# Kernel optimization log

Measured on AMD Instinct MI355X. Metric: run time of the kernel, lower is better.

## Reference

```python
import jax, jax.numpy as jnp
import numpy as np

LN_EPS = 1e-5


def _layernorm_hd(x, gamma, beta):
    # normalize jointly over the last two dims (H, D), matching nn.LayerNorm((H, D))
    m = jnp.mean(x, axis=(-2, -1), keepdims=True)
    v = jnp.var(x, axis=(-2, -1), keepdims=True)
    return (x - m) * jax.lax.rsqrt(v + LN_EPS) * gamma + beta


def setup_inputs() -> dict:
    B, S, H, D = 4, 4096, 8, 64
    key = jax.random.key(0)
    k1, k2, k3 = jax.random.split(key, 3)
    heads_input = jax.random.normal(k1, (B, S, H, D), dtype=jnp.float32)
    W_hid = jax.random.normal(k2, (2 * D, 3 * D), dtype=jnp.float32) * (1.0 / np.sqrt(2 * D))
    b_hid = jnp.zeros((3 * D,), dtype=jnp.float32)
    W_og = jax.random.normal(k3, (2 * D, D), dtype=jnp.float32) * (1.0 / np.sqrt(2 * D))
    b_og = jnp.zeros((D,), dtype=jnp.float32)
    ln_gamma = jnp.ones((H, D), dtype=jnp.float32)
    ln_beta = jnp.zeros((H, D), dtype=jnp.float32)
    init_cx = jnp.zeros((H, D), dtype=jnp.float32)
    return {"heads_input": heads_input, "W_hid": W_hid, "b_hid": b_hid,
            "W_og": W_og, "b_og": b_og, "ln_gamma": ln_gamma,
            "ln_beta": ln_beta, "init_cx": init_cx}


def reference(heads_input, W_hid, b_hid, W_og, b_og, ln_gamma, ln_beta, init_cx):
    B, S, H, D = heads_input.shape
    # RS1cumsumFunc: exclusive (right-shifted) cumsum along seq of detached input
    x_det = jax.lax.stop_gradient(heads_input)
    cs = jnp.cumsum(x_det, axis=1)
    csum_raw = jnp.concatenate([jnp.zeros_like(cs[:, :1]), cs[:, :-1]], axis=1)
    csum = _layernorm_hd(csum_raw, ln_gamma, ln_beta)

    # trans_hid on concat(heads_input, csum): [B,S,H,2D] -> [B,S,H,3D]
    hid_in = jnp.concatenate([heads_input, csum], axis=-1)
    h3 = jnp.einsum('bshd,de->bshe', hid_in, W_hid) + b_hid
    igate, fgate, hidden = jnp.split(h3, 3, axis=-1)
    fg = jax.nn.sigmoid(fgate)
    igh = jax.nn.sigmoid(igate) * jax.nn.relu(hidden)

    # LGateFunc: cell_t = fg_t * cell_{t-1} + igh_t, cell_{-1} = init_cx
    def combine(c1, c2):
        a1, b1 = c1
        a2, b2 = c2
        return a1 * a2, b1 * a2 + b2

    a, b = jax.lax.associative_scan(combine, (fg, igh), axis=1)
    cell = a * init_cx + b  # init_cx [H,D] broadcasts over [B,S,H,D]

    og_in = jnp.concatenate([heads_input, cell], axis=-1)
    og = jax.nn.sigmoid(jnp.einsum('bshd,de->bshe', og_in, W_og) + b_og)
    return og * cell
```

## Files before the change

### kernel.cpp

```cpp
#include <hip/hip_runtime.h>
#include <math.h>

#define S_   4096
#define H_   8
#define D_   64
#define HD_  512
#define NCH  256
#define LCH  16
#define RC   128

typedef __bf16 bf16x8 __attribute__((ext_vector_type(8)));
typedef float  f32x4  __attribute__((ext_vector_type(4)));

__device__ __forceinline__ float sigm(float v) { return 1.f / (1.f + __expf(-v)); }

__global__ __launch_bounds__(256) void k_wt(const float* __restrict__ Wh,
                                            const float* __restrict__ Wo,
                                            __bf16* __restrict__ Wth,
                                            __bf16* __restrict__ Wto) {
  int idx = blockIdx.x * 256 + threadIdx.x;
  if (idx < 24576) {
    int k = idx / 192, n = idx % 192;
    Wth[n * 128 + k] = (__bf16)Wh[idx];
  } else {
    int j = idx - 24576;
    int k = j >> 6, n = j & 63;
    Wto[n * 128 + k] = (__bf16)Wo[j];
  }
}

__global__ __launch_bounds__(512) void k_chunk_sums(const float* __restrict__ x,
                                                    float* __restrict__ sums) {
  const int b = blockIdx.x >> 8, c = blockIdx.x & 255;
  const int t = threadIdx.x;
  const float* p = x + ((size_t)b * S_ + c * LCH) * HD_ + t;
  float acc = 0.f;
  #pragma unroll
  for (int i = 0; i < LCH; ++i) acc += p[(size_t)i * HD_];
  sums[((size_t)b * NCH + c) * HD_ + t] = acc;
}

__global__ __launch_bounds__(512) void k_scan_offsets(float* __restrict__ sums) {
  const int b = blockIdx.x, t = threadIdx.x;
  float run = 0.f;
  for (int c = 0; c < NCH; ++c) {
    size_t idx = ((size_t)b * NCH + c) * HD_ + t;
    float v = sums[idx];
    sums[idx] = run;
    run += v;
  }
}

__global__ __launch_bounds__(512) void k_ln(const float* __restrict__ x,
                                            const float* __restrict__ offs,
                                            const float* __restrict__ gamma,
                                            const float* __restrict__ beta,
                                            __bf16* __restrict__ Abf) {
  __shared__ float2 red[2][8];
  const int b = blockIdx.x >> 8, c = blockIdx.x & 255;
  const int t = threadIdx.x;
  float run = offs[((size_t)b * NCH + c) * HD_ + t];
  const float g = gamma[t], be = beta[t];
  const size_t xbase = ((size_t)b * S_ + c * LCH) * HD_ + t;
  const int h = t >> 6, d = t & 63;
  float xv = x[xbase];
  for (int i = 0; i < LCH; ++i) {
    float xn = (i < LCH - 1) ? x[xbase + (size_t)(i + 1) * HD_] : 0.f;
    float v = run, v2 = run * run;
    #pragma unroll
    for (int o = 32; o; o >>= 1) { v += __shfl_xor(v, o); v2 += __shfl_xor(v2, o); }
    if ((t & 63) == 0) red[i & 1][t >> 6] = make_float2(v, v2);
    __syncthreads();
    float s1 = 0.f, s2 = 0.f;
    #pragma unroll
    for (int w = 0; w < 8; ++w) { s1 += red[i & 1][w].x; s2 += red[i & 1][w].y; }
    float m = s1 * (1.f / HD_);
    float var = fmaf(-m, m, s2 * (1.f / HD_));
    float inv = rsqrtf(var + 1e-5f);
    size_t r = ((size_t)b * S_ + c * LCH + i) * H_ + h;
    Abf[r * 128 + 64 + d] = (__bf16)((run - m) * inv * g + be);
    Abf[r * 128 + d] = (__bf16)xv;
    run += xv;
    xv = xn;
  }
}

__global__ __launch_bounds__(256) void k_gates(const __bf16* __restrict__ Abf,
                                               const __bf16* __restrict__ Wt,
                                               const float* __restrict__ bh,
                                               float* __restrict__ fg,
                                               float* __restrict__ igh,
                                               float* __restrict__ cA,
                                               float* __restrict__ cB) {
  __shared__ float fgl[RC * 68];
  __shared__ float ighl[RC * 68];
  const int t = threadIdx.x;
  const int wave = t >> 6, lane = t & 63;
  const int quad = lane >> 4, l16 = lane & 15;
  const int r0 = blockIdx.x * RC;

  f32x4 acc[2][12];
  #pragma unroll
  for (int i = 0; i < 2; ++i)
    #pragma unroll
    for (int j = 0; j < 12; ++j) acc[i][j] = (f32x4){0.f, 0.f, 0.f, 0.f};

  #pragma unroll
  for (int ks = 0; ks < 4; ++ks) {
    bf16x8 bfrag[12];
    #pragma unroll
    for (int nt = 0; nt < 12; ++nt)
      bfrag[nt] = *(const bf16x8*)(Wt + (nt * 16 + l16) * 128 + ks * 32 + quad * 8);
    #pragma unroll
    for (int mi = 0; mi < 2; ++mi) {
      int mt = wave * 2 + mi;
      bf16x8 afrag = *(const bf16x8*)(Abf + (size_t)(r0 + mt * 16 + l16) * 128 + ks * 32 + quad * 8);
      #pragma unroll
      for (int nt = 0; nt < 12; ++nt)
        acc[mi][nt] = __builtin_amdgcn_mfma_f32_16x16x32_bf16(afrag, bfrag[nt], acc[mi][nt], 0, 0, 0);
    }
  }

  #pragma unroll
  for (int mi = 0; mi < 2; ++mi) {
    int mt = wave * 2 + mi;
    #pragma unroll
    for (int nt = 0; nt < 4; ++nt) {
      int d = nt * 16 + l16;
      float bi = bh[d], bf = bh[64 + d], bhv = bh[128 + d];
      #pragma unroll
      for (int r = 0; r < 4; ++r) {
        int row = mt * 16 + quad * 4 + r;
        float ip = acc[mi][nt][r] + bi;
        float fp = acc[mi][nt + 4][r] + bf;
        float hp = acc[mi][nt + 8][r] + bhv;
        fgl[row * 68 + d] = sigm(fp);
        ighl[row * 68 + d] = sigm(ip) * fmaxf(hp, 0.f);
      }
    }
  }
  __syncthreads();

  #pragma unroll
  for (int rep = 0; rep < 8; ++rep) {
    int idx = rep * 256 + t;
    int row = idx >> 4, c4 = idx & 15;
    float4 vf = *(const float4*)&fgl[row * 68 + c4 * 4];
    float4 vg = *(const float4*)&ighl[row * 68 + c4 * 4];
    ((float4*)fg)[(size_t)(r0 + row) * 16 + c4] = vf;
    ((float4*)igh)[(size_t)(r0 + row) * 16 + c4] = vg;
  }

  #pragma unroll
  for (int p = 0; p < 2; ++p) {
    int hd = p * 256 + t;
    int h = hd >> 6, d = hd & 63;
    float a = 1.f, bb = 0.f;
    #pragma unroll
    for (int s = 0; s < LCH; ++s) {
      float f = fgl[(s * 8 + h) * 68 + d];
      float g = ighl[(s * 8 + h) * 68 + d];
      a *= f;
      bb = fmaf(bb, f, g);
    }
    cA[(size_t)blockIdx.x * 512 + hd] = a;
    cB[(size_t)blockIdx.x * 512 + hd] = bb;
  }
}

__global__ __launch_bounds__(512) void k_cell_scan(float* __restrict__ cA,
                                                   const float* __restrict__ cB,
                                                   const float* __restrict__ initcx) {
  const int b = blockIdx.x, t = threadIdx.x;
  float run = initcx[t];
  for (int c = 0; c < NCH; ++c) {
    size_t idx = ((size_t)b * NCH + c) * HD_ + t;
    float a = cA[idx], bb = cB[idx];
    cA[idx] = run;
    run = fmaf(a, run, bb);
  }
}

__global__ __launch_bounds__(256) void k_og(const __bf16* __restrict__ Abf,
                                            const float* __restrict__ fg,
                                            const float* __restrict__ igh,
                                            const float* __restrict__ cin,
                                            const __bf16* __restrict__ Wt,
                                            const float* __restrict__ bo,
                                            float* __restrict__ out) {
  __shared__ float cl[RC * 68];
  const int t = threadIdx.x;
  const int wave = t >> 6, lane = t & 63;
  const int quad = lane >> 4, l16 = lane & 15;
  const int r0 = blockIdx.x * RC;

  #pragma unroll
  for (int p = 0; p < 2; ++p) {
    int hd = p * 256 + t;
    int h = hd >> 6, d = hd & 63;
    float run = cin[(size_t)blockIdx.x * 512 + hd];
    #pragma unroll
    for (int s = 0; s < LCH; ++s) {
      size_t row = (size_t)r0 + s * 8 + h;
      run = fmaf(fg[row * 64 + d], run, igh[row * 64 + d]);
      cl[(s * 8 + h) * 68 + d] = run;
    }
  }
  __syncthreads();

  f32x4 acc[2][4];
  #pragma unroll
  for (int i = 0; i < 2; ++i)
    #pragma unroll
    for (int j = 0; j < 4; ++j) acc[i][j] = (f32x4){0.f, 0.f, 0.f, 0.f};

  #pragma unroll
  for (int ks = 0; ks < 4; ++ks) {
    bf16x8 bfrag[4];
    #pragma unroll
    for (int nt = 0; nt < 4; ++nt)
      bfrag[nt] = *(const bf16x8*)(Wt + (nt * 16 + l16) * 128 + ks * 32 + quad * 8);
    #pragma unroll
    for (int mi = 0; mi < 2; ++mi) {
      int mt = wave * 2 + mi;
      bf16x8 afrag;
      if (ks < 2) {
        afrag = *(const bf16x8*)(Abf + (size_t)(r0 + mt * 16 + l16) * 128 + ks * 32 + quad * 8);
      } else {
        int rowl = mt * 16 + l16;
        const float* src = &cl[rowl * 68 + (ks - 2) * 32 + quad * 8];
        #pragma unroll
        for (int j = 0; j < 8; ++j) afrag[j] = (__bf16)src[j];
      }
      #pragma unroll
      for (int nt = 0; nt < 4; ++nt)
        acc[mi][nt] = __builtin_amdgcn_mfma_f32_16x16x32_bf16(afrag, bfrag[nt], acc[mi][nt], 0, 0, 0);
    }
  }

  #pragma unroll
  for (int mi = 0; mi < 2; ++mi) {
    int mt = wave * 2 + mi;
    #pragma unroll
    for (int nt = 0; nt < 4; ++nt) {
      int d = nt * 16 + l16;
      float bv = bo[d];
      #pragma unroll
      for (int r = 0; r < 4; ++r) {
        int rowl = mt * 16 + quad * 4 + r;
        float og = sigm(acc[mi][nt][r] + bv);
        out[(size_t)(r0 + rowl) * 64 + d] = og * cl[rowl * 68 + d];
      }
    }
  }
}

extern "C" void kernel_launch(void* const* d_in, const int* in_sizes, int n_in,
                              void* d_out, int out_size, void* d_ws, size_t ws_size,
                              hipStream_t stream) {
  const float* x      = (const float*)d_in[0];
  const float* W_hid  = (const float*)d_in[1];
  const float* b_hid  = (const float*)d_in[2];
  const float* W_og   = (const float*)d_in[3];
  const float* b_og   = (const float*)d_in[4];
  const float* gamma  = (const float*)d_in[5];
  const float* beta   = (const float*)d_in[6];
  const float* initcx = (const float*)d_in[7];
  float* out = (float*)d_out;
  float* ws  = (float*)d_ws;

  float*  buf0 = ws;
  float*  buf1 = ws + 524288;
  __bf16* Abf  = (__bf16*)(ws + 1048576);
  float*  fgv  = ws + 1048576 + 8388608;
  float*  ighv = fgv + 8388608;
  __bf16* Wth  = (__bf16*)(ighv + 8388608);
  __bf16* Wto  = Wth + 24576;

  k_wt         <<<128,  256, 0, stream>>>(W_hid, W_og, Wth, Wto);
  k_chunk_sums <<<1024, 512, 0, stream>>>(x, buf0);
  k_scan_offsets<<<4,   512, 0, stream>>>(buf0);
  k_ln         <<<1024, 512, 0, stream>>>(x, buf0, gamma, beta, Abf);
  k_gates      <<<1024, 256, 0, stream>>>(Abf, Wth, b_hid, fgv, ighv, buf0, buf1);
  k_cell_scan  <<<4,    512, 0, stream>>>(buf0, buf1, initcx);
  k_og         <<<1024, 256, 0, stream>>>(Abf, fgv, ighv, buf0, Wto, b_og, out);
}
```

Measured before the change: 219.0 us.

## Recompute gates in output kernel instead of storing fg/igh to global memory

```diff
diff --git a/kernel.cpp b/kernel.cpp
--- a/kernel.cpp
+++ b/kernel.cpp
@@ -29,43 +29,49 @@
   }
 }
 
-__global__ __launch_bounds__(512) void k_chunk_sums(const float* __restrict__ x,
-                                                    float* __restrict__ sums) {
-  const int b = blockIdx.x >> 8, c = blockIdx.x & 255;
+__global__ __launch_bounds__(512) void k_pre(const float* __restrict__ x,
+                                             float* __restrict__ sums,
+                                             __bf16* __restrict__ Abf) {
   const int t = threadIdx.x;
-  const float* p = x + ((size_t)b * S_ + c * LCH) * HD_ + t;
+  const int h = t >> 6, d = t & 63;
+  const size_t r0 = (size_t)blockIdx.x * RC;
+  const float* p = x + r0 * 64 + t;
   float acc = 0.f;
   #pragma unroll
-  for (int i = 0; i < LCH; ++i) acc += p[(size_t)i * HD_];
-  sums[((size_t)b * NCH + c) * HD_ + t] = acc;
-}
-
-__global__ __launch_bounds__(512) void k_scan_offsets(float* __restrict__ sums) {
+  for (int i = 0; i < LCH; ++i) {
+    float v = p[(size_t)i * HD_];
+    acc += v;
+    Abf[(r0 + (size_t)i * H_ + h) * 128 + d] = (__bf16)v;
+  }
+  sums[(size_t)blockIdx.x * HD_ + t] = acc;
+}
+
+__global__ __launch_bounds__(512) void k_scan_offsets(const float* __restrict__ sums,
+                                                      float* __restrict__ offs) {
   const int b = blockIdx.x, t = threadIdx.x;
   float run = 0.f;
+  #pragma unroll 16
   for (int c = 0; c < NCH; ++c) {
     size_t idx = ((size_t)b * NCH + c) * HD_ + t;
     float v = sums[idx];
-    sums[idx] = run;
+    offs[idx] = run;
     run += v;
   }
 }
 
-__global__ __launch_bounds__(512) void k_ln(const float* __restrict__ x,
-                                            const float* __restrict__ offs,
+__global__ __launch_bounds__(512) void k_ln(const float* __restrict__ offs,
                                             const float* __restrict__ gamma,
                                             const float* __restrict__ beta,
                                             __bf16* __restrict__ Abf) {
   __shared__ float2 red[2][8];
-  const int b = blockIdx.x >> 8, c = blockIdx.x & 255;
   const int t = threadIdx.x;
-  float run = offs[((size_t)b * NCH + c) * HD_ + t];
+  const int h = t >> 6, d = t & 63;
+  const size_t r0 = (size_t)blockIdx.x * RC;
+  float run = offs[(size_t)blockIdx.x * HD_ + t];
   const float g = gamma[t], be = beta[t];
-  const size_t xbase = ((size_t)b * S_ + c * LCH) * HD_ + t;
-  const int h = t >> 6, d = t & 63;
-  float xv = x[xbase];
   for (int i = 0; i < LCH; ++i) {
-    float xn = (i < LCH - 1) ? x[xbase + (size_t)(i + 1) * HD_] : 0.f;
+    size_t row = r0 + (size_t)i * H_ + h;
+    float xv = (float)Abf[row * 128 + d];
     float v = run, v2 = run * run;
     #pragma unroll
     for (int o = 32; o; o >>= 1) { v += __shfl_xor(v, o); v2 += __shfl_xor(v2, o); }
@@ -77,27 +83,20 @@
     float m = s1 * (1.f / HD_);
     float var = fmaf(-m, m, s2 * (1.f / HD_));
     float inv = rsqrtf(var + 1e-5f);
-    size_t r = ((size_t)b * S_ + c * LCH + i) * H_ + h;
-    Abf[r * 128 + 64 + d] = (__bf16)((run - m) * inv * g + be);
-    Abf[r * 128 + d] = (__bf16)xv;
+    Abf[row * 128 + 64 + d] = (__bf16)((run - m) * inv * g + be);
     run += xv;
-    xv = xn;
   }
 }
 
 __global__ __launch_bounds__(256) void k_gates(const __bf16* __restrict__ Abf,
                                                const __bf16* __restrict__ Wt,
                                                const float* __restrict__ bh,
-                                               float* __restrict__ fg,
-                                               float* __restrict__ igh,
                                                float* __restrict__ cA,
                                                float* __restrict__ cB) {
-  __shared__ float fgl[RC * 68];
-  __shared__ float ighl[RC * 68];
   const int t = threadIdx.x;
   const int wave = t >> 6, lane = t & 63;
   const int quad = lane >> 4, l16 = lane & 15;
-  const int r0 = blockIdx.x * RC;
+  const size_t r0 = (size_t)blockIdx.x * RC;
 
   f32x4 acc[2][12];
   #pragma unroll
@@ -113,8 +112,8 @@
       bfrag[nt] = *(const bf16x8*)(Wt + (nt * 16 + l16) * 128 + ks * 32 + quad * 8);
     #pragma unroll
     for (int mi = 0; mi < 2; ++mi) {
-      int mt = wave * 2 + mi;
-      bf16x8 afrag = *(const bf16x8*)(Abf + (size_t)(r0 + mt * 16 + l16) * 128 + ks * 32 + quad * 8);
+      int h = wave * 2 + mi;
+      bf16x8 afrag = *(const bf16x8*)(Abf + (r0 + l16 * H_ + h) * 128 + ks * 32 + quad * 8);
       #pragma unroll
       for (int nt = 0; nt < 12; ++nt)
         acc[mi][nt] = __builtin_amdgcn_mfma_f32_16x16x32_bf16(afrag, bfrag[nt], acc[mi][nt], 0, 0, 0);
@@ -123,133 +122,159 @@
 
   #pragma unroll
   for (int mi = 0; mi < 2; ++mi) {
-    int mt = wave * 2 + mi;
+    int h = wave * 2 + mi;
     #pragma unroll
     for (int nt = 0; nt < 4; ++nt) {
       int d = nt * 16 + l16;
       float bi = bh[d], bf = bh[64 + d], bhv = bh[128 + d];
+      float A = 1.f, Bv = 0.f;
       #pragma unroll
       for (int r = 0; r < 4; ++r) {
-        int row = mt * 16 + quad * 4 + r;
-        float ip = acc[mi][nt][r] + bi;
-        float fp = acc[mi][nt + 4][r] + bf;
-        float hp = acc[mi][nt + 8][r] + bhv;
-        fgl[row * 68 + d] = sigm(fp);
-        ighl[row * 68 + d] = sigm(ip) * fmaxf(hp, 0.f);
-      }
-    }
-  }
-  __syncthreads();
-
-  #pragma unroll
-  for (int rep = 0; rep < 8; ++rep) {
-    int idx = rep * 256 + t;
-    int row = idx >> 4, c4 = idx & 15;
-    float4 vf = *(const float4*)&fgl[row * 68 + c4 * 4];
-    float4 vg = *(const float4*)&ighl[row * 68 + c4 * 4];
-    ((float4*)fg)[(size_t)(r0 + row) * 16 + c4] = vf;
-    ((float4*)igh)[(size_t)(r0 + row) * 16 + c4] = vg;
-  }
-
-  #pragma unroll
-  for (int p = 0; p < 2; ++p) {
-    int hd = p * 256 + t;
-    int h = hd >> 6, d = hd & 63;
-    float a = 1.f, bb = 0.f;
-    #pragma unroll
-    for (int s = 0; s < LCH; ++s) {
-      float f = fgl[(s * 8 + h) * 68 + d];
-      float g = ighl[(s * 8 + h) * 68 + d];
-      a *= f;
-      bb = fmaf(bb, f, g);
-    }
-    cA[(size_t)blockIdx.x * 512 + hd] = a;
-    cB[(size_t)blockIdx.x * 512 + hd] = bb;
-  }
-}
-
-__global__ __launch_bounds__(512) void k_cell_scan(float* __restrict__ cA,
+        float f = sigm(acc[mi][nt + 4][r] + bf);
+        float g = sigm(acc[mi][nt][r] + bi) * fmaxf(acc[mi][nt + 8][r] + bhv, 0.f);
+        A = f * A;
+        Bv = fmaf(f, Bv, g);
+      }
+      float At = 0.f, Bt = 0.f;
+      #pragma unroll
+      for (int q = 0; q < 4; ++q) {
+        float Aq = __shfl(A, q * 16 + l16);
+        float Bq = __shfl(Bv, q * 16 + l16);
+        if (q == 0) { At = Aq; Bt = Bq; }
+        else { At = Aq * At; Bt = fmaf(Aq, Bt, Bq); }
+      }
+      if (quad == 0) {
+        cA[(size_t)blockIdx.x * HD_ + h * 64 + d] = At;
+        cB[(size_t)blockIdx.x * HD_ + h * 64 + d] = Bt;
+      }
+    }
+  }
+}
+
+__global__ __launch_bounds__(512) void k_cell_scan(const float* __restrict__ cA,
                                                    const float* __restrict__ cB,
-                                                   const float* __restrict__ initcx) {
+                                                   const float* __restrict__ initcx,
+                                                   float* __restrict__ cin) {
   const int b = blockIdx.x, t = threadIdx.x;
   float run = initcx[t];
+  #pragma unroll 16
   for (int c = 0; c < NCH; ++c) {
     size_t idx = ((size_t)b * NCH + c) * HD_ + t;
     float a = cA[idx], bb = cB[idx];
-    cA[idx] = run;
+    cin[idx] = run;
     run = fmaf(a, run, bb);
   }
 }
 
 __global__ __launch_bounds__(256) void k_og(const __bf16* __restrict__ Abf,
-                                            const float* __restrict__ fg,
-                                            const float* __restrict__ igh,
+                                            const __bf16* __restrict__ Wth,
+                                            const float* __restrict__ bh,
+                                            const __bf16* __restrict__ Wto,
+                                            const float* __restrict__ bo,
                                             const float* __restrict__ cin,
-                                            const __bf16* __restrict__ Wt,
-                                            const float* __restrict__ bo,
                                             float* __restrict__ out) {
   __shared__ float cl[RC * 68];
   const int t = threadIdx.x;
   const int wave = t >> 6, lane = t & 63;
   const int quad = lane >> 4, l16 = lane & 15;
-  const int r0 = blockIdx.x * RC;
-
-  #pragma unroll
-  for (int p = 0; p < 2; ++p) {
-    int hd = p * 256 + t;
-    int h = hd >> 6, d = hd & 63;
-    float run = cin[(size_t)blockIdx.x * 512 + hd];
-    #pragma unroll
-    for (int s = 0; s < LCH; ++s) {
-      size_t row = (size_t)r0 + s * 8 + h;
-      run = fmaf(fg[row * 64 + d], run, igh[row * 64 + d]);
-      cl[(s * 8 + h) * 68 + d] = run;
+  const size_t r0 = (size_t)blockIdx.x * RC;
+
+  f32x4 acc[2][12];
+  #pragma unroll
+  for (int i = 0; i < 2; ++i)
+    #pragma unroll
+    for (int j = 0; j < 12; ++j) acc[i][j] = (f32x4){0.f, 0.f, 0.f, 0.f};
+
+  #pragma unroll
+  for (int ks = 0; ks < 4; ++ks) {
+    bf16x8 bfrag[12];
+    #pragma unroll
+    for (int nt = 0; nt < 12; ++nt)
+      bfrag[nt] = *(const bf16x8*)(Wth + (nt * 16 + l16) * 128 + ks * 32 + quad * 8);
+    #pragma unroll
+    for (int mi = 0; mi < 2; ++mi) {
+      int h = wave * 2 + mi;
+      bf16x8 afrag = *(const bf16x8*)(Abf + (r0 + l16 * H_ + h) * 128 + ks * 32 + quad * 8);
+      #pragma unroll
+      for (int nt = 0; nt < 12; ++nt)
+        acc[mi][nt] = __builtin_amdgcn_mfma_f32_16x16x32_bf16(afrag, bfrag[nt], acc[mi][nt], 0, 0, 0);
+    }
+  }
+
+  #pragma unroll
+  for (int mi = 0; mi < 2; ++mi) {
+    int h = wave * 2 + mi;
+    #pragma unroll
+    for (int nt = 0; nt < 4; ++nt) {
+      int d = nt * 16 + l16;
+      float bi = bh[d], bf = bh[64 + d], bhv = bh[128 + d];
+      float fr[4], gr[4];
+      float A = 1.f, Bv = 0.f;
+      #pragma unroll
+      for (int r = 0; r < 4; ++r) {
+        fr[r] = sigm(acc[mi][nt + 4][r] + bf);
+        gr[r] = sigm(acc[mi][nt][r] + bi) * fmaxf(acc[mi][nt + 8][r] + bhv, 0.f);
+        A = fr[r] * A;
+        Bv = fmaf(fr[r], Bv, gr[r]);
+      }
+      float c = cin[(size_t)blockIdx.x * HD_ + h * 64 + d];
+      #pragma unroll
+      for (int q = 0; q < 3; ++q) {
+        float Aq = __shfl(A, q * 16 + l16);
+        float Bq = __shfl(Bv, q * 16 + l16);
+        if (q < quad) c = fmaf(Aq, c, Bq);
+      }
+      #pragma unroll
+      for (int r = 0; r < 4; ++r) {
+        c = fmaf(fr[r], c, gr[r]);
+        cl[(h * 16 + quad * 4 + r) * 68 + d] = c;
+      }
     }
   }
   __syncthreads();
 
-  f32x4 acc[2][4];
+  f32x4 acc2[2][4];
   #pragma unroll
   for (int i = 0; i < 2; ++i)
     #pragma unroll
-    for (int j = 0; j < 4; ++j) acc[i][j] = (f32x4){0.f, 0.f, 0.f, 0.f};
+    for (int j = 0; j < 4; ++j) acc2[i][j] = (f32x4){0.f, 0.f, 0.f, 0.f};
 
   #pragma unroll
   for (int ks = 0; ks < 4; ++ks) {
     bf16x8 bfrag[4];
     #pragma unroll
     for (int nt = 0; nt < 4; ++nt)
-      bfrag[nt] = *(const bf16x8*)(Wt + (nt * 16 + l16) * 128 + ks * 32 + quad * 8);
+      bfrag[nt] = *(const bf16x8*)(Wto + (nt * 16 + l16) * 128 + ks * 32 + quad * 8);
     #pragma unroll
     for (int mi = 0; mi < 2; ++mi) {
-      int mt = wave * 2 + mi;
+      int h = wave * 2 + mi;
       bf16x8 afrag;
       if (ks < 2) {
-        afrag = *(const bf16x8*)(Abf + (size_t)(r0 + mt * 16 + l16) * 128 + ks * 32 + quad * 8);
+        afrag = *(const bf16x8*)(Abf + (r0 + l16 * H_ + h) * 128 + ks * 32 + quad * 8);
       } else {
-        int rowl = mt * 16 + l16;
-        const float* src = &cl[rowl * 68 + (ks - 2) * 32 + quad * 8];
+        const float* src = &cl[(h * 16 + l16) * 68 + (ks - 2) * 32 + quad * 8];
         #pragma unroll
         for (int j = 0; j < 8; ++j) afrag[j] = (__bf16)src[j];
       }
       #pragma unroll
       for (int nt = 0; nt < 4; ++nt)
-        acc[mi][nt] = __builtin_amdgcn_mfma_f32_16x16x32_bf16(afrag, bfrag[nt], acc[mi][nt], 0, 0, 0);
+        acc2[mi][nt] = __builtin_amdgcn_mfma_f32_16x16x32_bf16(afrag, bfrag[nt], acc2[mi][nt], 0, 0, 0);
     }
   }
 
   #pragma unroll
   for (int mi = 0; mi < 2; ++mi) {
-    int mt = wave * 2 + mi;
+    int h = wave * 2 + mi;
     #pragma unroll
     for (int nt = 0; nt < 4; ++nt) {
       int d = nt * 16 + l16;
       float bv = bo[d];
       #pragma unroll
       for (int r = 0; r < 4; ++r) {
-        int rowl = mt * 16 + quad * 4 + r;
-        float og = sigm(acc[mi][nt][r] + bv);
-        out[(size_t)(r0 + rowl) * 64 + d] = og * cl[rowl * 68 + d];
+        int s = quad * 4 + r;
+        float og = sigm(acc2[mi][nt][r] + bv);
+        float cv = cl[(h * 16 + s) * 68 + d];
+        out[(r0 + (size_t)s * H_ + h) * 64 + d] = og * cv;
       }
     }
   }
@@ -269,19 +294,21 @@
   float* out = (float*)d_out;
   float* ws  = (float*)d_ws;
 
-  float*  buf0 = ws;
-  float*  buf1 = ws + 524288;
-  __bf16* Abf  = (__bf16*)(ws + 1048576);
-  float*  fgv  = ws + 1048576 + 8388608;
-  float*  ighv = fgv + 8388608;
-  __bf16* Wth  = (__bf16*)(ighv + 8388608);
+  const size_t SM = 524288;
+  float*  sums = ws;
+  float*  offs = sums + SM;
+  float*  cA   = offs + SM;
+  float*  cB   = cA + SM;
+  float*  cin  = cB + SM;
+  __bf16* Abf  = (__bf16*)(cin + SM);
+  __bf16* Wth  = (__bf16*)(Abf + (size_t)131072 * 128);
   __bf16* Wto  = Wth + 24576;
 
-  k_wt         <<<128,  256, 0, stream>>>(W_hid, W_og, Wth, Wto);
-  k_chunk_sums <<<1024, 512, 0, stream>>>(x, buf0);
-  k_scan_offsets<<<4,   512, 0, stream>>>(buf0);
-  k_ln         <<<1024, 512, 0, stream>>>(x, buf0, gamma, beta, Abf);
-  k_gates      <<<1024, 256, 0, stream>>>(Abf, Wth, b_hid, fgv, ighv, buf0, buf1);
-  k_cell_scan  <<<4,    512, 0, stream>>>(buf0, buf1, initcx);
-  k_og         <<<1024, 256, 0, stream>>>(Abf, fgv, ighv, buf0, Wto, b_og, out);
-}
+  k_wt          <<<128,  256, 0, stream>>>(W_hid, W_og, Wth, Wto);
+  k_pre         <<<1024, 512, 0, stream>>>(x, sums, Abf);
+  k_scan_offsets<<<4,    512, 0, stream>>>(sums, offs);
+  k_ln          <<<1024, 512, 0, stream>>>(offs, gamma, beta, Abf);
+  k_gates       <<<1024, 256, 0, stream>>>(Abf, Wth, b_hid, cA, cB);
+  k_cell_scan   <<<4,    512, 0, stream>>>(cA, cB, initcx, cin);
+  k_og          <<<1024, 256, 0, stream>>>(Abf, Wth, b_hid, Wto, b_og, cin, out);
+}
```

Result: slower. 257.0 us (+17.4%).
